# Kernel tuning notes

Hardware: AMD Instinct MI355X
Metric: run time of the kernel (lower is better)

The kernel has to match this reference:

```python
import jax, jax.numpy as jnp
import numpy as np

EMB = 16      # importance embedding channels (ch 0 = logit, 1: = cov features)
NSEG = 196    # n_segments (14x14 superpixel grid)
MC = 16       # num_monte_carlo
TEMP = 1.0    # initial Gumbel/RelaxedBernoulli temperature (compute_temperature(0))
JITTER = 1e-3 # numerical_stability_check: diagonal jitter so Cholesky succeeds


def setup_inputs() -> dict:
    key = jax.random.key(0)
    k1, k2, k3 = jax.random.split(key, 3)
    B, C, H, W = 16, 3, 224, 224
    x = jax.random.normal(k1, (B, C, H, W), jnp.float32)
    groups = jax.random.randint(k2, (B, H, W), 0, NSEG, jnp.int32)
    W_conv = jax.random.normal(k3, (EMB, C), jnp.float32) * 0.1
    b_conv = jnp.zeros((EMB,), jnp.float32)
    return {"x": x, "groups": groups, "W_conv": W_conv, "b_conv": b_conv}


def _group_mean(groups, emb):
    # scatter_reduce(mean, include_self=False): per-batch segment mean, 0 for empty groups
    # emb: [B,E,H,W], groups: [B,H,W] -> [B, NSEG, E]
    B, E, H, W = emb.shape
    flat = emb.reshape(B, E, H * W).transpose(0, 2, 1).reshape(B * H * W, E)
    ids = (groups.reshape(B, H * W).astype(jnp.int32)
           + NSEG * jnp.arange(B, dtype=jnp.int32)[:, None]).reshape(-1)
    sums = jax.ops.segment_sum(flat, ids, num_segments=B * NSEG).reshape(B, NSEG, E)
    cnt = jax.ops.segment_sum(jnp.ones((B * H * W,), flat.dtype), ids,
                              num_segments=B * NSEG).reshape(B, NSEG, 1)
    return sums / jnp.maximum(cnt, 1.0)


def reference(x, groups, W_conv, b_conv):
    B, C, H, W = x.shape
    # importance_predictor as 1x1 conv: [B,C,H,W] -> [B,EMB,H,W]
    emb = jnp.einsum('bchw,ec->behw', x, W_conv) + b_conv[None, :, None, None]

    avg = _group_mean(groups, emb)            # [B, NSEG, EMB]
    mu = avg[:, :, 0]                          # [B, NSEG]
    gemb = avg[:, :, 1:]                       # [B, NSEG, EMB-1]
    # groups_emb.mT @ groups_emb (groups_emb is [B, EMB-1, NSEG] in torch)
    sigma = jnp.einsum('bse,bte->bst', gemb, gemb)
    sigma = sigma + JITTER * jnp.eye(NSEG, dtype=sigma.dtype)

    pixel_probs = jax.nn.sigmoid(emb[:, 0])    # [B, H, W]
    group_probs = jax.nn.sigmoid(mu)           # [B, NSEG]

    # MultivariateNormal(mu, sigma).rsample([MC]).movedim(0,-1)
    L = jnp.linalg.cholesky(sigma)             # [B, NSEG, NSEG]
    kg, ku = jax.random.split(jax.random.key(42))
    eps = jax.random.normal(kg, (B, NSEG, MC), x.dtype)
    logits_mc = mu[:, :, None] + jnp.einsum('bst,btm->bsm', L, eps)  # [B,NSEG,MC]

    # RelaxedBernoulli(temp, probs=sigmoid(logits_mc)).rsample()
    u = jax.random.uniform(ku, (B, NSEG, MC), x.dtype, 1e-6, 1.0 - 1e-6)
    logistic = jnp.log(u) - jnp.log1p(-u)
    relaxed = jax.nn.sigmoid((logits_mc + logistic) / TEMP)
    hard = (relaxed > 0.5).astype(relaxed.dtype)
    groups_mcmc = hard + relaxed - jax.lax.stop_gradient(relaxed)  # straight-through

    # groups_to_mask: gather group decision back to every pixel
    gf = groups.reshape(B, H * W).astype(jnp.int32)
    idx = jnp.broadcast_to(gf[:, :, None], (B, H * W, MC))
    mask = jnp.take_along_axis(groups_mcmc, idx, axis=1)           # [B, HW, MC]
    mask = mask.reshape(B, H, W, MC)
    mask = jnp.broadcast_to(mask[:, None], (B, C, H, W, MC))       # expand channels
    return mask, group_probs, pixel_probs, sigma
```

## Files before the change

kernel.cpp:

```cpp
#include <hip/hip_runtime.h>
#include <stdint.h>

#define HW    50176
#define BATCH 16
#define NSEG  196
#define EMB   16
#define MC    16
#define JITTER 0.001f
#define EBLK  14
#define PXB   3584

__host__ __device__ inline void threefry2x32(uint32_t k0, uint32_t k1,
                                             uint32_t x0, uint32_t x1,
                                             uint32_t& o0, uint32_t& o1) {
  uint32_t k2 = k0 ^ k1 ^ 0x1BD11BDAu;
#define TFR(r) { x0 += x1; x1 = (x1 << (r)) | (x1 >> (32 - (r))); x1 ^= x0; }
  x0 += k0; x1 += k1;
  TFR(13) TFR(15) TFR(26) TFR(6)
  x0 += k1; x1 += k2 + 1u;
  TFR(17) TFR(29) TFR(16) TFR(24)
  x0 += k2; x1 += k0 + 2u;
  TFR(13) TFR(15) TFR(26) TFR(6)
  x0 += k0; x1 += k1 + 3u;
  TFR(17) TFR(29) TFR(16) TFR(24)
  x0 += k1; x1 += k2 + 4u;
  TFR(13) TFR(15) TFR(26) TFR(6)
  x0 += k2; x1 += k0 + 5u;
#undef TFR
  o0 = x0; o1 = x1;
}

__device__ inline float erfinv_f32(float x) {
  float w = -log1pf(-x * x);
  float p;
  if (w < 5.0f) {
    w = w - 2.5f;
    p = 2.81022636e-08f;
    p = 3.43273939e-07f + p * w;
    p = -3.5233877e-06f + p * w;
    p = -4.39150654e-06f + p * w;
    p = 0.00021858087f + p * w;
    p = -0.00125372503f + p * w;
    p = -0.00417768164f + p * w;
    p = 0.246640727f + p * w;
    p = 1.50140941f + p * w;
  } else {
    w = sqrtf(w) - 3.0f;
    p = -0.000200214257f;
    p = 0.000100950558f + p * w;
    p = 0.00134934322f + p * w;
    p = -0.00367342844f + p * w;
    p = 0.00573950773f + p * w;
    p = -0.0076224613f + p * w;
    p = 0.00943887047f + p * w;
    p = 1.00167406f + p * w;
    p = 2.83297682f + p * w;
  }
  return p * x;
}

__device__ inline float bits_to_f01(uint32_t bits) {
  uint32_t fb = (bits >> 9) | 0x3F800000u;
  return __uint_as_float(fb) - 1.0f;
}

__global__ __launch_bounds__(256) void emb_kernel(
    const float* __restrict__ x, const int* __restrict__ groups,
    const float* __restrict__ Wc, const float* __restrict__ bc,
    float* __restrict__ partial, float* __restrict__ pixel_probs) {
  __shared__ float lsum[4 * NSEG];
  int b = blockIdx.x / EBLK;
  int blk = blockIdx.x % EBLK;
  int tid = threadIdx.x;
  for (int i = tid; i < 4 * NSEG; i += 256) lsum[i] = 0.0f;
  __syncthreads();
  const float* xb = x + (size_t)b * 3 * HW;
  float w0 = Wc[0], w1 = Wc[1], w2 = Wc[2], b0 = bc[0];
  for (int k = 0; k < PXB / 256; ++k) {
    int p = blk * PXB + k * 256 + tid;
    float x0 = xb[p], x1 = xb[HW + p], x2 = xb[2 * HW + p];
    int g = groups[b * HW + p];
    float e = w0 * x0 + w1 * x1;
    e = e + w2 * x2 + b0;
    pixel_probs[b * HW + p] = 1.0f / (1.0f + expf(-e));
    atomicAdd(&lsum[g], x0);
    atomicAdd(&lsum[NSEG + g], x1);
    atomicAdd(&lsum[2 * NSEG + g], x2);
    atomicAdd(&lsum[3 * NSEG + g], 1.0f);
  }
  __syncthreads();
  float* pb = partial + (size_t)blockIdx.x * (4 * NSEG);
  if (tid < NSEG) {
#pragma unroll
    for (int c = 0; c < 4; ++c) pb[c * NSEG + tid] = lsum[c * NSEG + tid];
  }
}

__global__ __launch_bounds__(256, 1) void fused_kernel(
    const float* __restrict__ partial, const float* __restrict__ Wc,
    const float* __restrict__ bc,
    uint32_t kg0, uint32_t kg1, uint32_t ku0, uint32_t ku1,
    float* __restrict__ group_probs, float* __restrict__ sigma_out,
    float* __restrict__ hard) {
  int b = blockIdx.x;
  int tid = threadIdx.x;
  int lane = tid & 63;
  int wave = tid >> 6;
  __shared__ float ge[15][NSEG];
  __shared__ float mu_l[NSEG];
  __shared__ float eps_lds[NSEG * MC];
  __shared__ __align__(16) float piv[2][16];

  for (int t = tid; t < NSEG * MC; t += 256) {
    uint32_t a0, a1;
    threefry2x32(kg0, kg1, 0u, (uint32_t)(b * NSEG * MC + t), a0, a1);
    float f = bits_to_f01(a0 ^ a1);
    const float lo = -0.99999994f;
    float u = fmaxf(lo, f * (1.0f - lo) + lo);
    eps_lds[t] = 1.4142135623730951f * erfinv_f32(u);
  }

  if (tid < NSEG) {
    float sx0 = 0.0f, sx1 = 0.0f, sx2 = 0.0f, cn = 0.0f;
    for (int bb = 0; bb < EBLK; ++bb) {
      const float* pb = partial + (size_t)(b * EBLK + bb) * (4 * NSEG);
      sx0 += pb[tid]; sx1 += pb[NSEG + tid];
      sx2 += pb[2 * NSEG + tid]; cn += pb[3 * NSEG + tid];
    }
    float denom = fmaxf(cn, 1.0f);
#pragma unroll
    for (int j = 0; j < EMB; ++j) {
      float e = Wc[j * 3 + 0] * sx0 + Wc[j * 3 + 1] * sx1;
      e = e + Wc[j * 3 + 2] * sx2 + bc[j] * cn;
      float v = e / denom;
      if (j == 0) {
        mu_l[tid] = v;
        group_probs[b * NSEG + tid] = 1.0f / (1.0f + expf(-v));
      } else {
        ge[j - 1][tid] = v;
      }
    }
  }
  __syncthreads();

  if (tid < NSEG) {
    int t = tid;
    float gt[15];
#pragma unroll
    for (int j = 0; j < 15; ++j) gt[j] = ge[j][t];
    for (int s = 0; s < NSEG; ++s) {
      float a = 0.0f;
#pragma unroll
      for (int j = 0; j < 15; ++j) a = fmaf(ge[j][s], gt[j], a);
      if (s == t) a += JITTER;
      sigma_out[((size_t)b * NSEG + s) * NSEG + t] = a;
    }
  }

  int i = tid;
  float g[15];
#pragma unroll
  for (int j = 0; j < 15; ++j) g[j] = (i < NSEG) ? ge[j][i] : 0.0f;
  float acc[16];
#pragma unroll
  for (int m = 0; m < 16; ++m) acc[m] = 0.0f;
  if (tid == 0) {
#pragma unroll
    for (int j = 0; j < 15; ++j) piv[0][j] = g[j];
    piv[0][15] = 0.0f;
  }
  __syncthreads();

  const float sj = 0.031622776601683794f;
  for (int k = 0; k < NSEG; ++k) {
    const float* pv = piv[k & 1];
    float4 p0 = *(const float4*)(pv);
    float4 p1 = *(const float4*)(pv + 4);
    float4 p2 = *(const float4*)(pv + 8);
    float4 p3 = *(const float4*)(pv + 12);
    float gk[15] = {p0.x, p0.y, p0.z, p0.w, p1.x, p1.y, p1.z, p1.w,
                    p2.x, p2.y, p2.z, p2.w, p3.x, p3.y, p3.z};
    float t0 = fmaf(gk[0], gk[0], JITTER);
    float t1 = gk[1] * gk[1];   float t2 = gk[2] * gk[2];
    float t3 = gk[3] * gk[3];   float t4 = gk[4] * gk[4];
    float t5 = gk[5] * gk[5];   float t6 = gk[6] * gk[6];
    float t7 = gk[7] * gk[7];   float t8 = gk[8] * gk[8];
    float t9 = gk[9] * gk[9];   float t10 = gk[10] * gk[10];
    float t11 = gk[11] * gk[11]; float t12 = gk[12] * gk[12];
    float t13 = gk[13] * gk[13]; float t14 = gk[14] * gk[14];
    float u0 = t0 + t1, u1 = t2 + t3, u2 = t4 + t5, u3 = t6 + t7;
    float u4 = t8 + t9, u5 = t10 + t11, u6 = t12 + t13;
    float v0 = u0 + u1, v1 = u2 + u3, v2 = u4 + u5, v3 = u6 + t14;
    float jn = (v0 + v1) + (v2 + v3);
    float invd = __builtin_amdgcn_rsqf(jn);
    float dd = jn * invd;
    float beta = (invd * invd) * __builtin_amdgcn_rcpf(fmaf(sj, invd, 1.0f));

    int s0 = k >> 6;
    if (wave >= s0) {
      const float4* ep = (const float4*)(eps_lds + k * MC);
      float4 e0 = ep[0], e1 = ep[1], e2 = ep[2], e3 = ep[3];
      float ek[16] = {e0.x, e0.y, e0.z, e0.w, e1.x, e1.y, e1.z, e1.w,
                      e2.x, e2.y, e2.z, e2.w, e3.x, e3.y, e3.z, e3.w};
      float dot = 0.0f;
#pragma unroll
      for (int j = 0; j < 15; ++j) dot = fmaf(g[j], gk[j], dot);
      float w;
      if (wave == s0) {
        int owner = k & 63;
        w = (lane > owner) ? dot * invd : ((lane == owner) ? dd : 0.0f);
      } else {
        w = dot * invd;
      }
#pragma unroll
      for (int m = 0; m < 16; ++m) acc[m] = fmaf(w, ek[m], acc[m]);
      float bd = beta * dot;
#pragma unroll
      for (int j = 0; j < 15; ++j) g[j] = fmaf(-bd, gk[j], g[j]);
      int kn = k + 1;
      if (kn < NSEG && i == kn) {
        float* pw = piv[kn & 1];
#pragma unroll
        for (int j = 0; j < 15; ++j) pw[j] = g[j];
      }
    }
    __syncthreads();
  }

  if (i < NSEG) {
    float mui = mu_l[i];
    float4 outv[4];
    float* op = (float*)outv;
#pragma unroll
    for (int m = 0; m < 16; ++m) {
      uint32_t a0, a1;
      threefry2x32(ku0, ku1, 0u, (uint32_t)(b * NSEG * MC + i * MC + m), a0, a1);
      float f = bits_to_f01(a0 ^ a1);
      const float mn = 1e-6f;
      const float mx = (float)(1.0 - 1e-6);
      float uu = fmaxf(mn, f * (mx - mn) + mn);
      float lg = logf(uu) - log1pf(-uu);
      float z = mui + acc[m] + lg;
      op[m] = (z > 0.0f) ? 1.0f : 0.0f;
    }
    float4* hp = (float4*)(hard + ((size_t)b * NSEG + i) * MC);
#pragma unroll
    for (int q = 0; q < 4; ++q) hp[q] = outv[q];
  }
}

__global__ __launch_bounds__(256) void mask_kernel(
    const int* __restrict__ groups, const float* __restrict__ hard,
    float4* __restrict__ out) {
  int f = blockIdx.x * blockDim.x + threadIdx.x;
  if (f >= BATCH * 3 * HW * 4) return;
  int pix = f >> 2;
  int q = f & 3;
  int b = pix / (3 * HW);
  int p = pix % HW;
  int g = groups[b * HW + p];
  out[f] = ((const float4*)hard)[(b * NSEG + g) * 4 + q];
}

extern "C" void kernel_launch(void* const* d_in, const int* in_sizes, int n_in,
                              void* d_out, int out_size, void* d_ws, size_t ws_size,
                              hipStream_t stream) {
  const float* x = (const float*)d_in[0];
  const int* groups = (const int*)d_in[1];
  const float* Wc = (const float*)d_in[2];
  const float* bc = (const float*)d_in[3];

  float* out = (float*)d_out;
  float* mask_out = out;
  float* gp_out = out + 38535168;
  float* pp_out = gp_out + 3136;
  float* sig_out = pp_out + 802816;

  float* ws = (float*)d_ws;
  float* partial = ws;
  float* hard    = ws + 175616;

  emb_kernel<<<BATCH * EBLK, 256, 0, stream>>>(x, groups, Wc, bc, partial, pp_out);

  uint32_t kg0, kg1, ku0, ku1;
  threefry2x32(0u, 42u, 0u, 0u, kg0, kg1);
  threefry2x32(0u, 42u, 0u, 1u, ku0, ku1);

  fused_kernel<<<BATCH, 256, 0, stream>>>(partial, Wc, bc, kg0, kg1, ku0, ku1,
                                          gp_out, sig_out, hard);
  mask_kernel<<<(BATCH * 3 * HW * 4 + 255) / 256, 256, 0, stream>>>(
      groups, hard, (float4*)mask_out);
}
```

Measured before the change: 272.7 us.

## Block Cholesky panels per wave with readlane pivots, cutting per-step barriers

```diff
diff --git a/kernel.cpp b/kernel.cpp
--- a/kernel.cpp
+++ b/kernel.cpp
@@ -64,6 +64,10 @@
   return __uint_as_float(fb) - 1.0f;
 }
 
+__device__ inline float readlane_f(float v, int lane) {
+  return __int_as_float(__builtin_amdgcn_readlane(__float_as_int(v), lane));
+}
+
 __global__ __launch_bounds__(256) void emb_kernel(
     const float* __restrict__ x, const int* __restrict__ groups,
     const float* __restrict__ Wc, const float* __restrict__ bc,
@@ -109,7 +113,7 @@
   __shared__ float ge[15][NSEG];
   __shared__ float mu_l[NSEG];
   __shared__ float eps_lds[NSEG * MC];
-  __shared__ __align__(16) float piv[2][16];
+  __shared__ __align__(16) float pbuf[2][64][20];
 
   for (int t = tid; t < NSEG * MC; t += 256) {
     uint32_t a0, a1;
@@ -164,68 +168,88 @@
   float acc[16];
 #pragma unroll
   for (int m = 0; m < 16; ++m) acc[m] = 0.0f;
-  if (tid == 0) {
-#pragma unroll
-    for (int j = 0; j < 15; ++j) piv[0][j] = g[j];
-    piv[0][15] = 0.0f;
-  }
   __syncthreads();
 
   const float sj = 0.031622776601683794f;
-  for (int k = 0; k < NSEG; ++k) {
-    const float* pv = piv[k & 1];
-    float4 p0 = *(const float4*)(pv);
-    float4 p1 = *(const float4*)(pv + 4);
-    float4 p2 = *(const float4*)(pv + 8);
-    float4 p3 = *(const float4*)(pv + 12);
-    float gk[15] = {p0.x, p0.y, p0.z, p0.w, p1.x, p1.y, p1.z, p1.w,
-                    p2.x, p2.y, p2.z, p2.w, p3.x, p3.y, p3.z};
-    float t0 = fmaf(gk[0], gk[0], JITTER);
-    float t1 = gk[1] * gk[1];   float t2 = gk[2] * gk[2];
-    float t3 = gk[3] * gk[3];   float t4 = gk[4] * gk[4];
-    float t5 = gk[5] * gk[5];   float t6 = gk[6] * gk[6];
-    float t7 = gk[7] * gk[7];   float t8 = gk[8] * gk[8];
-    float t9 = gk[9] * gk[9];   float t10 = gk[10] * gk[10];
-    float t11 = gk[11] * gk[11]; float t12 = gk[12] * gk[12];
-    float t13 = gk[13] * gk[13]; float t14 = gk[14] * gk[14];
-    float u0 = t0 + t1, u1 = t2 + t3, u2 = t4 + t5, u3 = t6 + t7;
-    float u4 = t8 + t9, u5 = t10 + t11, u6 = t12 + t13;
-    float v0 = u0 + u1, v1 = u2 + u3, v2 = u4 + u5, v3 = u6 + t14;
-    float jn = (v0 + v1) + (v2 + v3);
-    float invd = __builtin_amdgcn_rsqf(jn);
-    float dd = jn * invd;
+
+#define SCALAR_CHAIN()                                                      \
+    float t0 = fmaf(gk[0], gk[0], JITTER);                                  \
+    float t1 = gk[1] * gk[1];   float t2 = gk[2] * gk[2];                   \
+    float t3 = gk[3] * gk[3];   float t4 = gk[4] * gk[4];                   \
+    float t5 = gk[5] * gk[5];   float t6 = gk[6] * gk[6];                   \
+    float t7 = gk[7] * gk[7];   float t8 = gk[8] * gk[8];                   \
+    float t9 = gk[9] * gk[9];   float t10 = gk[10] * gk[10];                \
+    float t11 = gk[11] * gk[11]; float t12 = gk[12] * gk[12];               \
+    float t13 = gk[13] * gk[13]; float t14 = gk[14] * gk[14];               \
+    float u0 = t0 + t1, u1 = t2 + t3, u2 = t4 + t5, u3 = t6 + t7;           \
+    float u4 = t8 + t9, u5 = t10 + t11, u6 = t12 + t13;                     \
+    float v0 = u0 + u1, v1 = u2 + u3, v2 = u4 + u5, v3 = u6 + t14;          \
+    float jn = (v0 + v1) + (v2 + v3);                                       \
+    float invd = __builtin_amdgcn_rsqf(jn);                                 \
+    float dd = jn * invd;                                                   \
     float beta = (invd * invd) * __builtin_amdgcn_rcpf(fmaf(sj, invd, 1.0f));
 
-    int s0 = k >> 6;
-    if (wave >= s0) {
-      const float4* ep = (const float4*)(eps_lds + k * MC);
-      float4 e0 = ep[0], e1 = ep[1], e2 = ep[2], e3 = ep[3];
-      float ek[16] = {e0.x, e0.y, e0.z, e0.w, e1.x, e1.y, e1.z, e1.w,
-                      e2.x, e2.y, e2.z, e2.w, e3.x, e3.y, e3.z, e3.w};
-      float dot = 0.0f;
-#pragma unroll
-      for (int j = 0; j < 15; ++j) dot = fmaf(g[j], gk[j], dot);
-      float w;
-      if (wave == s0) {
-        int owner = k & 63;
-        w = (lane > owner) ? dot * invd : ((lane == owner) ? dd : 0.0f);
-      } else {
-        w = dot * invd;
+  for (int P = 0; P < 4; ++P) {
+    const int kbase = P * 64;
+    const int plen = (P == 3) ? (NSEG - 192) : 64;
+    if (wave == P) {
+      for (int kk = 0; kk < plen; ++kk) {
+        int owner = kk;
+        float gk[15];
+#pragma unroll
+        for (int j = 0; j < 15; ++j) gk[j] = readlane_f(g[j], owner);
+        SCALAR_CHAIN()
+        if (lane == 0) {
+          float* pw = &pbuf[P & 1][kk][0];
+#pragma unroll
+          for (int j = 0; j < 15; ++j) pw[j] = gk[j];
+          pw[15] = invd;
+          pw[16] = beta;
+        }
+        const float4* ep = (const float4*)(eps_lds + (kbase + kk) * MC);
+        float4 e0 = ep[0], e1 = ep[1], e2 = ep[2], e3 = ep[3];
+        float ek[16] = {e0.x, e0.y, e0.z, e0.w, e1.x, e1.y, e1.z, e1.w,
+                        e2.x, e2.y, e2.z, e2.w, e3.x, e3.y, e3.z, e3.w};
+        float dot = 0.0f;
+#pragma unroll
+        for (int j = 0; j < 15; ++j) dot = fmaf(g[j], gk[j], dot);
+        float w = (lane > owner) ? dot * invd : ((lane == owner) ? dd : 0.0f);
+#pragma unroll
+        for (int m = 0; m < 16; ++m) acc[m] = fmaf(w, ek[m], acc[m]);
+        float bd = beta * dot;
+#pragma unroll
+        for (int j = 0; j < 15; ++j) g[j] = fmaf(-bd, gk[j], g[j]);
       }
-#pragma unroll
-      for (int m = 0; m < 16; ++m) acc[m] = fmaf(w, ek[m], acc[m]);
-      float bd = beta * dot;
-#pragma unroll
-      for (int j = 0; j < 15; ++j) g[j] = fmaf(-bd, gk[j], g[j]);
-      int kn = k + 1;
-      if (kn < NSEG && i == kn) {
-        float* pw = piv[kn & 1];
-#pragma unroll
-        for (int j = 0; j < 15; ++j) pw[j] = g[j];
+    }
+    __syncthreads();
+    if (wave > P) {
+      for (int kk = 0; kk < plen; ++kk) {
+        const float* pv = &pbuf[P & 1][kk][0];
+        float4 p0 = *(const float4*)(pv);
+        float4 p1 = *(const float4*)(pv + 4);
+        float4 p2 = *(const float4*)(pv + 8);
+        float4 p3 = *(const float4*)(pv + 12);
+        float gk[15] = {p0.x, p0.y, p0.z, p0.w, p1.x, p1.y, p1.z, p1.w,
+                        p2.x, p2.y, p2.z, p2.w, p3.x, p3.y, p3.z};
+        float invd = p3.w;
+        float beta = pv[16];
+        const float4* ep = (const float4*)(eps_lds + (kbase + kk) * MC);
+        float4 e0 = ep[0], e1 = ep[1], e2 = ep[2], e3 = ep[3];
+        float ek[16] = {e0.x, e0.y, e0.z, e0.w, e1.x, e1.y, e1.z, e1.w,
+                        e2.x, e2.y, e2.z, e2.w, e3.x, e3.y, e3.z, e3.w};
+        float dot = 0.0f;
+#pragma unroll
+        for (int j = 0; j < 15; ++j) dot = fmaf(g[j], gk[j], dot);
+        float w = dot * invd;
+#pragma unroll
+        for (int m = 0; m < 16; ++m) acc[m] = fmaf(w, ek[m], acc[m]);
+        float bd = beta * dot;
+#pragma unroll
+        for (int j = 0; j < 15; ++j) g[j] = fmaf(-bd, gk[j], g[j]);
       }
     }
-    __syncthreads();
-  }
+  }
+#undef SCALAR_CHAIN
 
   if (i < NSEG) {
     float mui = mu_l[i];
```

Result: slower. 287.6 us (+5.5%).

## Split sigma into separate blocks and block Cholesky pivots by four

Applied to the files above, without the earlier changes.

```diff
diff --git a/kernel.cpp b/kernel.cpp
--- a/kernel.cpp
+++ b/kernel.cpp
@@ -64,6 +64,33 @@
   return __uint_as_float(fb) - 1.0f;
 }
 
+__device__ inline float dot15(const float a[15], const float b[15]) {
+  float d = 0.0f;
+#pragma unroll
+  for (int j = 0; j < 15; ++j) d = fmaf(a[j], b[j], d);
+  return d;
+}
+
+__device__ inline void pivot_scalars(const float gk[15], float& invd,
+                                     float& dd, float& beta) {
+  const float sj = 0.031622776601683794f;
+  float t0 = fmaf(gk[0], gk[0], JITTER);
+  float t1 = gk[1] * gk[1];   float t2 = gk[2] * gk[2];
+  float t3 = gk[3] * gk[3];   float t4 = gk[4] * gk[4];
+  float t5 = gk[5] * gk[5];   float t6 = gk[6] * gk[6];
+  float t7 = gk[7] * gk[7];   float t8 = gk[8] * gk[8];
+  float t9 = gk[9] * gk[9];   float t10 = gk[10] * gk[10];
+  float t11 = gk[11] * gk[11]; float t12 = gk[12] * gk[12];
+  float t13 = gk[13] * gk[13]; float t14 = gk[14] * gk[14];
+  float u0 = t0 + t1, u1 = t2 + t3, u2 = t4 + t5, u3 = t6 + t7;
+  float u4 = t8 + t9, u5 = t10 + t11, u6 = t12 + t13;
+  float v0 = u0 + u1, v1 = u2 + u3, v2 = u4 + u5, v3 = u6 + t14;
+  float jn = (v0 + v1) + (v2 + v3);
+  invd = __builtin_amdgcn_rsqf(jn);
+  dd = jn * invd;
+  beta = (invd * invd) * __builtin_amdgcn_rcpf(fmaf(sj, invd, 1.0f));
+}
+
 __global__ __launch_bounds__(256) void emb_kernel(
     const float* __restrict__ x, const int* __restrict__ groups,
     const float* __restrict__ Wc, const float* __restrict__ bc,
@@ -96,20 +123,57 @@
   }
 }
 
-__global__ __launch_bounds__(256, 1) void fused_kernel(
+__global__ __launch_bounds__(256, 1) void main_kernel(
     const float* __restrict__ partial, const float* __restrict__ Wc,
     const float* __restrict__ bc,
     uint32_t kg0, uint32_t kg1, uint32_t ku0, uint32_t ku1,
     float* __restrict__ group_probs, float* __restrict__ sigma_out,
     float* __restrict__ hard) {
-  int b = blockIdx.x;
+  int bid = blockIdx.x;
   int tid = threadIdx.x;
-  int lane = tid & 63;
-  int wave = tid >> 6;
+
+  if (bid < 112) {
+    int b = bid / 7;
+    int tile = bid % 7;
+    __shared__ float ge_s[15][NSEG];
+    if (tid < NSEG) {
+      float sx0 = 0.0f, sx1 = 0.0f, sx2 = 0.0f, cn = 0.0f;
+      for (int bb = 0; bb < EBLK; ++bb) {
+        const float* pb = partial + (size_t)(b * EBLK + bb) * (4 * NSEG);
+        sx0 += pb[tid]; sx1 += pb[NSEG + tid];
+        sx2 += pb[2 * NSEG + tid]; cn += pb[3 * NSEG + tid];
+      }
+      float denom = fmaxf(cn, 1.0f);
+#pragma unroll
+      for (int j = 1; j < EMB; ++j) {
+        float e = Wc[j * 3 + 0] * sx0 + Wc[j * 3 + 1] * sx1;
+        e = e + Wc[j * 3 + 2] * sx2 + bc[j] * cn;
+        ge_s[j - 1][tid] = e / denom;
+      }
+    }
+    __syncthreads();
+    if (tid < NSEG) {
+      int t = tid;
+      float gt[15];
+#pragma unroll
+      for (int j = 0; j < 15; ++j) gt[j] = ge_s[j][t];
+      for (int r = 0; r < 28; ++r) {
+        int s = tile * 28 + r;
+        float a = 0.0f;
+#pragma unroll
+        for (int j = 0; j < 15; ++j) a = fmaf(ge_s[j][s], gt[j], a);
+        if (s == t) a += JITTER;
+        sigma_out[((size_t)b * NSEG + s) * NSEG + t] = a;
+      }
+    }
+    return;
+  }
+
+  int b = bid - 112;
   __shared__ float ge[15][NSEG];
   __shared__ float mu_l[NSEG];
   __shared__ float eps_lds[NSEG * MC];
-  __shared__ __align__(16) float piv[2][16];
+  __shared__ __align__(16) float pbuf[2][4][16];
 
   for (int t = tid; t < NSEG * MC; t += 256) {
     uint32_t a0, a1;
@@ -143,20 +207,6 @@
   }
   __syncthreads();
 
-  if (tid < NSEG) {
-    int t = tid;
-    float gt[15];
-#pragma unroll
-    for (int j = 0; j < 15; ++j) gt[j] = ge[j][t];
-    for (int s = 0; s < NSEG; ++s) {
-      float a = 0.0f;
-#pragma unroll
-      for (int j = 0; j < 15; ++j) a = fmaf(ge[j][s], gt[j], a);
-      if (s == t) a += JITTER;
-      sigma_out[((size_t)b * NSEG + s) * NSEG + t] = a;
-    }
-  }
-
   int i = tid;
   float g[15];
 #pragma unroll
@@ -164,68 +214,106 @@
   float acc[16];
 #pragma unroll
   for (int m = 0; m < 16; ++m) acc[m] = 0.0f;
-  if (tid == 0) {
-#pragma unroll
-    for (int j = 0; j < 15; ++j) piv[0][j] = g[j];
-    piv[0][15] = 0.0f;
+  if (tid < 4) {
+    float* pw = &pbuf[0][tid][0];
+#pragma unroll
+    for (int j = 0; j < 15; ++j) pw[j] = g[j];
   }
   __syncthreads();
 
-  const float sj = 0.031622776601683794f;
-  for (int k = 0; k < NSEG; ++k) {
-    const float* pv = piv[k & 1];
-    float4 p0 = *(const float4*)(pv);
-    float4 p1 = *(const float4*)(pv + 4);
-    float4 p2 = *(const float4*)(pv + 8);
-    float4 p3 = *(const float4*)(pv + 12);
-    float gk[15] = {p0.x, p0.y, p0.z, p0.w, p1.x, p1.y, p1.z, p1.w,
-                    p2.x, p2.y, p2.z, p2.w, p3.x, p3.y, p3.z};
-    float t0 = fmaf(gk[0], gk[0], JITTER);
-    float t1 = gk[1] * gk[1];   float t2 = gk[2] * gk[2];
-    float t3 = gk[3] * gk[3];   float t4 = gk[4] * gk[4];
-    float t5 = gk[5] * gk[5];   float t6 = gk[6] * gk[6];
-    float t7 = gk[7] * gk[7];   float t8 = gk[8] * gk[8];
-    float t9 = gk[9] * gk[9];   float t10 = gk[10] * gk[10];
-    float t11 = gk[11] * gk[11]; float t12 = gk[12] * gk[12];
-    float t13 = gk[13] * gk[13]; float t14 = gk[14] * gk[14];
-    float u0 = t0 + t1, u1 = t2 + t3, u2 = t4 + t5, u3 = t6 + t7;
-    float u4 = t8 + t9, u5 = t10 + t11, u6 = t12 + t13;
-    float v0 = u0 + u1, v1 = u2 + u3, v2 = u4 + u5, v3 = u6 + t14;
-    float jn = (v0 + v1) + (v2 + v3);
-    float invd = __builtin_amdgcn_rsqf(jn);
-    float dd = jn * invd;
-    float beta = (invd * invd) * __builtin_amdgcn_rcpf(fmaf(sj, invd, 1.0f));
-
-    int s0 = k >> 6;
-    if (wave >= s0) {
-      const float4* ep = (const float4*)(eps_lds + k * MC);
-      float4 e0 = ep[0], e1 = ep[1], e2 = ep[2], e3 = ep[3];
-      float ek[16] = {e0.x, e0.y, e0.z, e0.w, e1.x, e1.y, e1.z, e1.w,
-                      e2.x, e2.y, e2.z, e2.w, e3.x, e3.y, e3.z, e3.w};
-      float dot = 0.0f;
-#pragma unroll
-      for (int j = 0; j < 15; ++j) dot = fmaf(g[j], gk[j], dot);
-      float w;
-      if (wave == s0) {
-        int owner = k & 63;
-        w = (lane > owner) ? dot * invd : ((lane == owner) ? dd : 0.0f);
-      } else {
-        w = dot * invd;
-      }
-#pragma unroll
-      for (int m = 0; m < 16; ++m) acc[m] = fmaf(w, ek[m], acc[m]);
-      float bd = beta * dot;
-#pragma unroll
-      for (int j = 0; j < 15; ++j) g[j] = fmaf(-bd, gk[j], g[j]);
-      int kn = k + 1;
-      if (kn < NSEG && i == kn) {
-        float* pw = piv[kn & 1];
-#pragma unroll
-        for (int j = 0; j < 15; ++j) pw[j] = g[j];
-      }
+#define APPLY_PIVOT(rv, invd_, dd_, beta_, K)                               \
+  {                                                                         \
+    float dot = dot15(g, rv);                                               \
+    float w = (i > (K)) ? dot * (invd_)                                     \
+                        : ((i == (K)) ? (dd_) : 0.0f);                      \
+    const float4* ep = (const float4*)(eps_lds + (K) * MC);                 \
+    float4 e0 = ep[0], e1 = ep[1], e2 = ep[2], e3 = ep[3];                  \
+    float ek[16] = {e0.x, e0.y, e0.z, e0.w, e1.x, e1.y, e1.z, e1.w,         \
+                    e2.x, e2.y, e2.z, e2.w, e3.x, e3.y, e3.z, e3.w};        \
+    _Pragma("unroll")                                                       \
+    for (int m = 0; m < 16; ++m) acc[m] = fmaf(w, ek[m], acc[m]);           \
+    float bd = (beta_) * dot;                                               \
+    _Pragma("unroll")                                                       \
+    for (int j = 0; j < 15; ++j) g[j] = fmaf(-bd, rv[j], g[j]);             \
+  }
+
+  for (int t49 = 0; t49 < 49; ++t49) {
+    const float* pb0 = &pbuf[t49 & 1][0][0];
+    float r0[15], r1[15], r2[15], r3[15];
+    {
+      float4 a0 = *(const float4*)(pb0 + 0);
+      float4 a1 = *(const float4*)(pb0 + 4);
+      float4 a2 = *(const float4*)(pb0 + 8);
+      float4 a3 = *(const float4*)(pb0 + 12);
+      r0[0]=a0.x; r0[1]=a0.y; r0[2]=a0.z; r0[3]=a0.w;
+      r0[4]=a1.x; r0[5]=a1.y; r0[6]=a1.z; r0[7]=a1.w;
+      r0[8]=a2.x; r0[9]=a2.y; r0[10]=a2.z; r0[11]=a2.w;
+      r0[12]=a3.x; r0[13]=a3.y; r0[14]=a3.z;
+      a0 = *(const float4*)(pb0 + 16); a1 = *(const float4*)(pb0 + 20);
+      a2 = *(const float4*)(pb0 + 24); a3 = *(const float4*)(pb0 + 28);
+      r1[0]=a0.x; r1[1]=a0.y; r1[2]=a0.z; r1[3]=a0.w;
+      r1[4]=a1.x; r1[5]=a1.y; r1[6]=a1.z; r1[7]=a1.w;
+      r1[8]=a2.x; r1[9]=a2.y; r1[10]=a2.z; r1[11]=a2.w;
+      r1[12]=a3.x; r1[13]=a3.y; r1[14]=a3.z;
+      a0 = *(const float4*)(pb0 + 32); a1 = *(const float4*)(pb0 + 36);
+      a2 = *(const float4*)(pb0 + 40); a3 = *(const float4*)(pb0 + 44);
+      r2[0]=a0.x; r2[1]=a0.y; r2[2]=a0.z; r2[3]=a0.w;
+      r2[4]=a1.x; r2[5]=a1.y; r2[6]=a1.z; r2[7]=a1.w;
+      r2[8]=a2.x; r2[9]=a2.y; r2[10]=a2.z; r2[11]=a2.w;
+      r2[12]=a3.x; r2[13]=a3.y; r2[14]=a3.z;
+      a0 = *(const float4*)(pb0 + 48); a1 = *(const float4*)(pb0 + 52);
+      a2 = *(const float4*)(pb0 + 56); a3 = *(const float4*)(pb0 + 60);
+      r3[0]=a0.x; r3[1]=a0.y; r3[2]=a0.z; r3[3]=a0.w;
+      r3[4]=a1.x; r3[5]=a1.y; r3[6]=a1.z; r3[7]=a1.w;
+      r3[8]=a2.x; r3[9]=a2.y; r3[10]=a2.z; r3[11]=a2.w;
+      r3[12]=a3.x; r3[13]=a3.y; r3[14]=a3.z;
+    }
+    float invd0, dd0, beta0, invd1, dd1, beta1;
+    float invd2, dd2, beta2, invd3, dd3, beta3;
+    pivot_scalars(r0, invd0, dd0, beta0);
+    {
+      float d = dot15(r1, r0); float bd = beta0 * d;
+#pragma unroll
+      for (int j = 0; j < 15; ++j) r1[j] = fmaf(-bd, r0[j], r1[j]);
+    }
+    pivot_scalars(r1, invd1, dd1, beta1);
+    {
+      float d = dot15(r2, r0); float bd = beta0 * d;
+#pragma unroll
+      for (int j = 0; j < 15; ++j) r2[j] = fmaf(-bd, r0[j], r2[j]);
+      d = dot15(r2, r1); bd = beta1 * d;
+#pragma unroll
+      for (int j = 0; j < 15; ++j) r2[j] = fmaf(-bd, r1[j], r2[j]);
+    }
+    pivot_scalars(r2, invd2, dd2, beta2);
+    {
+      float d = dot15(r3, r0); float bd = beta0 * d;
+#pragma unroll
+      for (int j = 0; j < 15; ++j) r3[j] = fmaf(-bd, r0[j], r3[j]);
+      d = dot15(r3, r1); bd = beta1 * d;
+#pragma unroll
+      for (int j = 0; j < 15; ++j) r3[j] = fmaf(-bd, r1[j], r3[j]);
+      d = dot15(r3, r2); bd = beta2 * d;
+#pragma unroll
+      for (int j = 0; j < 15; ++j) r3[j] = fmaf(-bd, r2[j], r3[j]);
+    }
+    pivot_scalars(r3, invd3, dd3, beta3);
+
+    int k0 = 4 * t49;
+    APPLY_PIVOT(r0, invd0, dd0, beta0, k0 + 0)
+    APPLY_PIVOT(r1, invd1, dd1, beta1, k0 + 1)
+    APPLY_PIVOT(r2, invd2, dd2, beta2, k0 + 2)
+    APPLY_PIVOT(r3, invd3, dd3, beta3, k0 + 3)
+
+    int nb = 4 * (t49 + 1);
+    if (i >= nb && i < nb + 4) {
+      float* pw = &pbuf[(t49 + 1) & 1][i - nb][0];
+#pragma unroll
+      for (int j = 0; j < 15; ++j) pw[j] = g[j];
     }
     __syncthreads();
   }
+#undef APPLY_PIVOT
 
   if (i < NSEG) {
     float mui = mu_l[i];
@@ -286,8 +374,8 @@
   threefry2x32(0u, 42u, 0u, 0u, kg0, kg1);
   threefry2x32(0u, 42u, 0u, 1u, ku0, ku1);
 
-  fused_kernel<<<BATCH, 256, 0, stream>>>(partial, Wc, bc, kg0, kg1, ku0, ku1,
-                                          gp_out, sig_out, hard);
+  main_kernel<<<128, 256, 0, stream>>>(partial, Wc, bc, kg0, kg1, ku0, ku1,
+                                       gp_out, sig_out, hard);
   mask_kernel<<<(BATCH * 3 * HW * 4 + 255) / 256, 256, 0, stream>>>(
       groups, hard, (float4*)mask_out);
 }
```

Measured after the change: 252.2 us, median of 2. 1.08x faster.
